# Kernel tuning notes

Hardware: AMD Instinct MI355X
Metric: run time of the kernel (lower is better)

## Reference

```python
import jax, jax.numpy as jnp
import numpy as np

EPS = 1e-8

def _cosine_weights(keys, M, reverse=False):
    # keys: (bs, r, W); M: (bs, W, N) -> softmax over slots of cosine sim, shape (bs, r, N)
    kn = keys / (jnp.linalg.norm(keys, axis=-1, keepdims=True) + EPS)
    Mn = M / (jnp.linalg.norm(M, axis=1, keepdims=True) + EPS)
    dist = jnp.einsum('brw,bwn->brn', kn, Mn)
    if reverse:
        dist = -dist
    return jax.nn.softmax(dist, axis=2)

def setup_inputs() -> dict:
    key = jax.random.key(0)
    ks = jax.random.split(key, 8)
    bs, W, N, R = 128, 256, 2048, 4
    return {
        'k_r': jax.random.normal(ks[0], (bs, R * W), jnp.float32),
        'm_t': jax.random.normal(ks[1], (bs, W), jnp.float32),
        'e_t': jax.random.normal(ks[2], (bs, W), jnp.float32),
        'm_erased': jax.random.normal(ks[3], (bs, 1, W), jnp.float32),
        'memory': jax.random.uniform(ks[4], (bs, W, N), jnp.float32),
        'gW': jax.random.normal(ks[5], (1, 2 * W), jnp.float32) * 0.05,
        'gb': jnp.zeros((1,), jnp.float32),
        'oW': jax.random.normal(ks[6], (W, 2 * W), jnp.float32) * 0.05,
        'ob': jnp.zeros((W,), jnp.float32),
    }

def reference(k_r, m_t, e_t, m_erased, memory, gW, gb, oW, ob):
    bs, W, N = memory.shape
    R = k_r.shape[1] // W
    read_keys = jnp.tanh(k_r.reshape(bs, R, W))
    write_m = jnp.tanh(m_t.reshape(bs, 1, W))            # m_t candidate (bs,1,W)
    erase_vec = jax.nn.softmax(e_t.reshape(bs, 1, W), axis=2)
    # MixGate(write_m, m_erased)
    cat = jnp.concatenate([write_m, m_erased], axis=-1)  # (bs,1,2W)
    g = jax.nn.sigmoid(jnp.einsum('biw,ow->bio', cat, gW) + gb)  # (bs,1,1)
    gated = jnp.concatenate([g * write_m, (1.0 - g) * m_erased], axis=-1)
    write_key = jax.nn.relu(jnp.einsum('biw,ow->bio', gated, oW) + ob)  # (bs,1,W)
    # content weighting with reversed (dissimilarity) cosine
    write_wt = _cosine_weights(write_key, memory, reverse=True)  # (bs,1,N)
    # M = M * (1 - et^T wt) + mt^T wt
    reset_gate = 1.0 - jnp.einsum('biw,bin->bwn', erase_vec, write_wt)
    M_new = memory * reset_gate + jnp.einsum('biw,bin->bwn', write_m, write_wt)
    # read
    read_wt = _cosine_weights(read_keys, M_new)          # (bs,R,N)
    m_read = jnp.einsum('brn,bwn->brw', read_wt, M_new)  # (bs,R,W)
    return (m_read, M_new, read_wt)
```

## Files before the change

kernel.cpp:

```cpp
#include <hip/hip_runtime.h>
#include <math.h>

#define EPS 1e-8f
#define BS 128
#define W 256
#define N 2048
#define R 4

using v4f = float __attribute__((ext_vector_type(4)));

__device__ inline float wave_sum(float v) {
#pragma unroll
    for (int o = 32; o > 0; o >>= 1) v += __shfl_xor(v, o, 64);
    return v;
}
__device__ inline float wave_max(float v) {
#pragma unroll
    for (int o = 32; o > 0; o >>= 1) v = fmaxf(v, __shfl_xor(v, o, 64));
    return v;
}

__global__ void k_prep(const float* __restrict__ k_r, const float* __restrict__ m_t,
                       const float* __restrict__ e_t, const float* __restrict__ m_er,
                       const float* __restrict__ gW, const float* __restrict__ gb,
                       const float* __restrict__ oW, const float* __restrict__ ob,
                       float* __restrict__ wm_o, float* __restrict__ er_o,
                       float* __restrict__ knw_o, float* __restrict__ knr_o) {
    int b = blockIdx.x, t = threadIdx.x;
    int lane = t & 63, wid = t >> 6;
    __shared__ float red[4];
    __shared__ float gated[2 * W];
    __shared__ float wk_s[W];

    float wm = tanhf(m_t[b * W + t]);
    float me = m_er[b * W + t];
    wm_o[b * W + t] = wm;

    float e = e_t[b * W + t];
    float mx = wave_max(e);
    if (lane == 0) red[wid] = mx;
    __syncthreads();
    mx = fmaxf(fmaxf(red[0], red[1]), fmaxf(red[2], red[3]));
    __syncthreads();
    float ex = expf(e - mx);
    float s = wave_sum(ex);
    if (lane == 0) red[wid] = s;
    __syncthreads();
    s = red[0] + red[1] + red[2] + red[3];
    __syncthreads();
    er_o[b * W + t] = ex / s;

    float p = wm * gW[t] + me * gW[W + t];
    float ps = wave_sum(p);
    if (lane == 0) red[wid] = ps;
    __syncthreads();
    ps = red[0] + red[1] + red[2] + red[3] + gb[0];
    __syncthreads();
    float g = 1.0f / (1.0f + expf(-ps));
    gated[t] = g * wm;
    gated[W + t] = (1.0f - g) * me;
    __syncthreads();

    const float4* g4 = (const float4*)gated;
    float4 g0 = g4[lane];
    float4 g1 = g4[64 + lane];
    for (int i = 0; i < 64; i++) {
        int o = wid * 64 + i;
        const float4* orow = (const float4*)(oW + (size_t)o * 2 * W);
        float4 w0 = orow[lane];
        float4 w1 = orow[64 + lane];
        float pp = w0.x * g0.x + w0.y * g0.y + w0.z * g0.z + w0.w * g0.w
                 + w1.x * g1.x + w1.y * g1.y + w1.z * g1.z + w1.w * g1.w;
        pp = wave_sum(pp);
        if (lane == 0) wk_s[o] = fmaxf(pp + ob[o], 0.0f);
    }
    __syncthreads();
    float wk = wk_s[t];
    float ss = wave_sum(wk * wk);
    if (lane == 0) red[wid] = ss;
    __syncthreads();
    ss = red[0] + red[1] + red[2] + red[3];
    __syncthreads();
    knw_o[b * W + t] = wk / (sqrtf(ss) + EPS);

    for (int r = 0; r < R; r++) {
        float rk = tanhf(k_r[(b * R + r) * W + t]);
        float s2 = wave_sum(rk * rk);
        if (lane == 0) red[wid] = s2;
        __syncthreads();
        s2 = red[0] + red[1] + red[2] + red[3];
        __syncthreads();
        knr_o[(b * R + r) * W + t] = rk / (sqrtf(s2) + EPS);
    }
}

__global__ void __launch_bounds__(256, 2)
k_wdist(const float* __restrict__ mem, const float* __restrict__ knw,
        float* __restrict__ dist) {
    int b = blockIdx.y;
    int t = threadIdx.x;
    int half = t >> 7, c = t & 127;
    int n4 = blockIdx.x * 128 + c;
    __shared__ float k[W];
    __shared__ float4 pdot[128], pss[128];
    k[t] = knw[b * W + t];
    __syncthreads();
    const float4* base = (const float4*)(mem + (size_t)b * W * N) + n4;
    float4 dot = make_float4(0.f, 0.f, 0.f, 0.f);
    float4 ss = make_float4(0.f, 0.f, 0.f, 0.f);
    int w0 = half * 128;
#pragma unroll 8
    for (int i = 0; i < 128; i++) {
        int w = w0 + i;
        float4 v = base[(size_t)w * (N / 4)];
        float kw = k[w];
        dot.x += kw * v.x; dot.y += kw * v.y; dot.z += kw * v.z; dot.w += kw * v.w;
        ss.x += v.x * v.x; ss.y += v.y * v.y; ss.z += v.z * v.z; ss.w += v.w * v.w;
    }
    if (half == 0) { pdot[c] = dot; pss[c] = ss; }
    __syncthreads();
    if (half == 1) {
        float4 od = pdot[c], os = pss[c];
        dot.x += od.x; dot.y += od.y; dot.z += od.z; dot.w += od.w;
        ss.x += os.x; ss.y += os.y; ss.z += os.z; ss.w += os.w;
        float4 o;
        o.x = -(dot.x / (sqrtf(ss.x) + EPS));
        o.y = -(dot.y / (sqrtf(ss.y) + EPS));
        o.z = -(dot.z / (sqrtf(ss.z) + EPS));
        o.w = -(dot.w / (sqrtf(ss.w) + EPS));
        ((float4*)(dist + (size_t)b * N))[n4] = o;
    }
}

__global__ void __launch_bounds__(256, 2)
k_update(const float* __restrict__ mem, const float* __restrict__ wdist,
         const float* __restrict__ er, const float* __restrict__ wm,
         const float* __restrict__ knr,
         float* __restrict__ Mnew, float* __restrict__ dist_raw) {
    int b = blockIdx.y;
    int t = threadIdx.x;
    int lane = t & 63, wid = t >> 6;
    int half = t >> 7, c = t & 127;
    int n4 = blockIdx.x * 128 + c;
    __shared__ float se[W], sw[W];
    __shared__ float4 skT[W];
    __shared__ float red[4];
    __shared__ float4 pd0[128], pd1[128], pd2[128], pd3[128], pssv[128];
    se[t] = er[b * W + t];
    sw[t] = wm[b * W + t];
    const float* kb = knr + (size_t)b * R * W;
    skT[t] = make_float4(kb[t], kb[W + t], kb[2 * W + t], kb[3 * W + t]);

    const float4* drow4 = (const float4*)(wdist + (size_t)b * N);
    float4 a0 = drow4[t];
    float4 a1 = drow4[256 + t];
    float mx = fmaxf(fmaxf(fmaxf(a0.x, a0.y), fmaxf(a0.z, a0.w)),
                     fmaxf(fmaxf(a1.x, a1.y), fmaxf(a1.z, a1.w)));
    mx = wave_max(mx);
    if (lane == 0) red[wid] = mx;
    __syncthreads();
    mx = fmaxf(fmaxf(red[0], red[1]), fmaxf(red[2], red[3]));
    __syncthreads();
    float sm = expf(a0.x - mx) + expf(a0.y - mx) + expf(a0.z - mx) + expf(a0.w - mx)
             + expf(a1.x - mx) + expf(a1.y - mx) + expf(a1.z - mx) + expf(a1.w - mx);
    sm = wave_sum(sm);
    if (lane == 0) red[wid] = sm;
    __syncthreads();
    sm = red[0] + red[1] + red[2] + red[3];
    float inv = 1.0f / sm;
    float4 dmine = drow4[n4];
    float4 wt;
    wt.x = expf(dmine.x - mx) * inv;
    wt.y = expf(dmine.y - mx) * inv;
    wt.z = expf(dmine.z - mx) * inv;
    wt.w = expf(dmine.w - mx) * inv;

    const float4* mb = (const float4*)(mem + (size_t)b * W * N) + n4;
    v4f* obv = (v4f*)(Mnew + (size_t)b * W * N) + n4;
    float4 ssv = make_float4(0.f, 0.f, 0.f, 0.f);
    float4 d0 = make_float4(0.f, 0.f, 0.f, 0.f);
    float4 d1 = make_float4(0.f, 0.f, 0.f, 0.f);
    float4 d2 = make_float4(0.f, 0.f, 0.f, 0.f);
    float4 d3 = make_float4(0.f, 0.f, 0.f, 0.f);
    int w0 = half * 128;
#pragma unroll 8
    for (int i = 0; i < 128; i++) {
        int w = w0 + i;
        float4 v = mb[(size_t)w * (N / 4)];
        float ew = se[w], mw = sw[w];
        float4 mn;
        mn.x = v.x + wt.x * (mw - v.x * ew);
        mn.y = v.y + wt.y * (mw - v.y * ew);
        mn.z = v.z + wt.z * (mw - v.z * ew);
        mn.w = v.w + wt.w * (mw - v.w * ew);
        v4f sv; sv[0] = mn.x; sv[1] = mn.y; sv[2] = mn.z; sv[3] = mn.w;
        __builtin_nontemporal_store(sv, obv + (size_t)w * (N / 4));
        ssv.x += mn.x * mn.x; ssv.y += mn.y * mn.y;
        ssv.z += mn.z * mn.z; ssv.w += mn.w * mn.w;
        float4 kv = skT[w];
        d0.x += kv.x * mn.x; d0.y += kv.x * mn.y; d0.z += kv.x * mn.z; d0.w += kv.x * mn.w;
        d1.x += kv.y * mn.x; d1.y += kv.y * mn.y; d1.z += kv.y * mn.z; d1.w += kv.y * mn.w;
        d2.x += kv.z * mn.x; d2.y += kv.z * mn.y; d2.z += kv.z * mn.z; d2.w += kv.z * mn.w;
        d3.x += kv.w * mn.x; d3.y += kv.w * mn.y; d3.z += kv.w * mn.z; d3.w += kv.w * mn.w;
    }
    if (half == 0) {
        pd0[c] = d0; pd1[c] = d1; pd2[c] = d2; pd3[c] = d3; pssv[c] = ssv;
    }
    __syncthreads();
    if (half == 1) {
        float4 q;
        q = pd0[c]; d0.x += q.x; d0.y += q.y; d0.z += q.z; d0.w += q.w;
        q = pd1[c]; d1.x += q.x; d1.y += q.y; d1.z += q.z; d1.w += q.w;
        q = pd2[c]; d2.x += q.x; d2.y += q.y; d2.z += q.z; d2.w += q.w;
        q = pd3[c]; d3.x += q.x; d3.y += q.y; d3.z += q.z; d3.w += q.w;
        q = pssv[c]; ssv.x += q.x; ssv.y += q.y; ssv.z += q.z; ssv.w += q.w;
        float4 ivn;
        ivn.x = 1.0f / (sqrtf(ssv.x) + EPS);
        ivn.y = 1.0f / (sqrtf(ssv.y) + EPS);
        ivn.z = 1.0f / (sqrtf(ssv.z) + EPS);
        ivn.w = 1.0f / (sqrtf(ssv.w) + EPS);
        float4* dr = (float4*)(dist_raw + (size_t)b * R * N);
        dr[0 * (N / 4) + n4] = make_float4(d0.x * ivn.x, d0.y * ivn.y, d0.z * ivn.z, d0.w * ivn.w);
        dr[1 * (N / 4) + n4] = make_float4(d1.x * ivn.x, d1.y * ivn.y, d1.z * ivn.z, d1.w * ivn.w);
        dr[2 * (N / 4) + n4] = make_float4(d2.x * ivn.x, d2.y * ivn.y, d2.z * ivn.z, d2.w * ivn.w);
        dr[3 * (N / 4) + n4] = make_float4(d3.x * ivn.x, d3.y * ivn.y, d3.z * ivn.z, d3.w * ivn.w);
    }
}

__global__ void __launch_bounds__(256, 2)
k_mread(const float* __restrict__ Mnew, const float* __restrict__ dist_raw,
        float* __restrict__ rwt_out, float* __restrict__ m_read) {
    int b = blockIdx.y;
    int w0 = blockIdx.x * 64;
    int t = threadIdx.x;
    int lane = t & 63, wid = t >> 6;

    __shared__ float rwt_s[R * N];
    __shared__ float redm[16], reds[16];
    __shared__ float part[64][2][4];

    const float4* drr = (const float4*)(dist_raw + (size_t)b * R * N);
    float4 a[R][2];
    float mxr[R], smr[R];
#pragma unroll
    for (int r = 0; r < R; r++) {
        a[r][0] = drr[r * 512 + t];
        a[r][1] = drr[r * 512 + 256 + t];
        float m0 = fmaxf(fmaxf(a[r][0].x, a[r][0].y), fmaxf(a[r][0].z, a[r][0].w));
        float m1 = fmaxf(fmaxf(a[r][1].x, a[r][1].y), fmaxf(a[r][1].z, a[r][1].w));
        float m = wave_max(fmaxf(m0, m1));
        if (lane == 0) redm[r * 4 + wid] = m;
    }
    __syncthreads();
#pragma unroll
    for (int r = 0; r < R; r++) {
        mxr[r] = fmaxf(fmaxf(redm[r * 4 + 0], redm[r * 4 + 1]),
                       fmaxf(redm[r * 4 + 2], redm[r * 4 + 3]));
        float4 e0, e1;
        e0.x = expf(a[r][0].x - mxr[r]); e0.y = expf(a[r][0].y - mxr[r]);
        e0.z = expf(a[r][0].z - mxr[r]); e0.w = expf(a[r][0].w - mxr[r]);
        e1.x = expf(a[r][1].x - mxr[r]); e1.y = expf(a[r][1].y - mxr[r]);
        e1.z = expf(a[r][1].z - mxr[r]); e1.w = expf(a[r][1].w - mxr[r]);
        a[r][0] = e0; a[r][1] = e1;
        float s = e0.x + e0.y + e0.z + e0.w + e1.x + e1.y + e1.z + e1.w;
        s = wave_sum(s);
        if (lane == 0) reds[r * 4 + wid] = s;
    }
    __syncthreads();
    float4* rs4 = (float4*)rwt_s;
#pragma unroll
    for (int r = 0; r < R; r++) {
        smr[r] = reds[r * 4 + 0] + reds[r * 4 + 1] + reds[r * 4 + 2] + reds[r * 4 + 3];
        float inv = 1.0f / smr[r];
        float4 o0, o1;
        o0.x = a[r][0].x * inv; o0.y = a[r][0].y * inv;
        o0.z = a[r][0].z * inv; o0.w = a[r][0].w * inv;
        o1.x = a[r][1].x * inv; o1.y = a[r][1].y * inv;
        o1.z = a[r][1].z * inv; o1.w = a[r][1].w * inv;
        rs4[r * 512 + t] = o0;
        rs4[r * 512 + 256 + t] = o1;
        if (blockIdx.x == 0) {
            float4* ro = (float4*)(rwt_out + (size_t)b * R * N);
            ro[r * 512 + t] = o0;
            ro[r * 512 + 256 + t] = o1;
        }
    }
    __syncthreads();

    int half = wid & 1, rowgrp = wid >> 1;
    int fbase = half * 256 + lane;

    float4 rw[R][4];
#pragma unroll
    for (int r = 0; r < R; r++)
#pragma unroll
        for (int k = 0; k < 4; k++) rw[r][k] = rs4[r * 512 + fbase + k * 64];

    const float* Mb = Mnew + (size_t)b * W * N;
#pragma unroll 4
    for (int wi = 0; wi < 32; wi++) {
        int wl = rowgrp * 32 + wi;
        const v4f* mrow = (const v4f*)(Mb + (size_t)(w0 + wl) * N);
        float4 v[4];
#pragma unroll
        for (int k = 0; k < 4; k++) {
            v4f vv = __builtin_nontemporal_load(mrow + fbase + k * 64);
            v[k].x = vv[0]; v[k].y = vv[1]; v[k].z = vv[2]; v[k].w = vv[3];
        }
        float a0 = 0.f, a1 = 0.f, a2 = 0.f, a3 = 0.f;
#pragma unroll
        for (int k = 0; k < 4; k++) {
            a0 += rw[0][k].x * v[k].x + rw[0][k].y * v[k].y + rw[0][k].z * v[k].z + rw[0][k].w * v[k].w;
            a1 += rw[1][k].x * v[k].x + rw[1][k].y * v[k].y + rw[1][k].z * v[k].z + rw[1][k].w * v[k].w;
            a2 += rw[2][k].x * v[k].x + rw[2][k].y * v[k].y + rw[2][k].z * v[k].z + rw[2][k].w * v[k].w;
            a3 += rw[3][k].x * v[k].x + rw[3][k].y * v[k].y + rw[3][k].z * v[k].z + rw[3][k].w * v[k].w;
        }
        a0 = wave_sum(a0);
        a1 = wave_sum(a1);
        a2 = wave_sum(a2);
        a3 = wave_sum(a3);
        if (lane == 0) {
            part[wl][half][0] = a0;
            part[wl][half][1] = a1;
            part[wl][half][2] = a2;
            part[wl][half][3] = a3;
        }
    }
    __syncthreads();
    int w = t >> 2, r = t & 3;
    float sres = part[w][0][r] + part[w][1][r];
    m_read[((size_t)b * R + r) * W + w0 + w] = sres;
}

extern "C" void kernel_launch(void* const* d_in, const int* in_sizes, int n_in,
                              void* d_out, int out_size, void* d_ws, size_t ws_size,
                              hipStream_t stream) {
    const float* k_r  = (const float*)d_in[0];
    const float* m_t  = (const float*)d_in[1];
    const float* e_t  = (const float*)d_in[2];
    const float* m_er = (const float*)d_in[3];
    const float* mem  = (const float*)d_in[4];
    const float* gW   = (const float*)d_in[5];
    const float* gb   = (const float*)d_in[6];
    const float* oW   = (const float*)d_in[7];
    const float* ob   = (const float*)d_in[8];

    float* out = (float*)d_out;
    float* m_read = out;
    float* Mnew   = out + (size_t)BS * R * W;
    float* rwt    = out + (size_t)BS * R * W + (size_t)BS * W * N;

    float* ws  = (float*)d_ws;
    float* wm  = ws;
    float* er  = ws + (size_t)BS * W;
    float* knw = ws + (size_t)2 * BS * W;
    float* knr = ws + (size_t)3 * BS * W;
    float* wdist = ws + (size_t)3 * BS * W + (size_t)BS * R * W;
    float* draw  = wdist + (size_t)BS * N;

    k_prep<<<BS, 256, 0, stream>>>(k_r, m_t, e_t, m_er, gW, gb, oW, ob, wm, er, knw, knr);
    k_wdist<<<dim3(4, BS), 256, 0, stream>>>(mem, knw, wdist);
    k_update<<<dim3(4, BS), 256, 0, stream>>>(mem, wdist, er, wm, knr, Mnew, draw);
    k_mread<<<dim3(4, BS), 256, 0, stream>>>(Mnew, draw, rwt, m_read);
}
```

Measured before the change: 250.4 us.

## Compute m_read from original memory via algebraic expansion of update

The read kernel now computes m_read from the original memory tensor rather than the freshly written Mnew. It uses the identity Mnew = M - er*(M·wt) + wm*wt and recomputes the write-weight softmax locally. This removes the kernel's dependence on Mnew but doubles the dot-product work and raises register and shared-memory use. Nontemporal loads are replaced with normal loads and the unroll factor is reduced.

```diff
diff --git a/kernel.cpp b/kernel.cpp
--- a/kernel.cpp
+++ b/kernel.cpp
@@ -228,7 +228,9 @@
 }
 
 __global__ void __launch_bounds__(256, 2)
-k_mread(const float* __restrict__ Mnew, const float* __restrict__ dist_raw,
+k_mread(const float* __restrict__ mem, const float* __restrict__ wdist_raw,
+        const float* __restrict__ dist_raw, const float* __restrict__ er_g,
+        const float* __restrict__ wm_g,
         float* __restrict__ rwt_out, float* __restrict__ m_read) {
     int b = blockIdx.y;
     int w0 = blockIdx.x * 64;
@@ -236,100 +238,127 @@
     int lane = t & 63, wid = t >> 6;
 
     __shared__ float rwt_s[R * N];
-    __shared__ float redm[16], reds[16];
-    __shared__ float part[64][2][4];
+    __shared__ float u_s[R * N];
+    __shared__ float redm[20], reds[20], redc[16];
+    __shared__ float part_a[64][2][4], part_b[64][2][4];
 
     const float4* drr = (const float4*)(dist_raw + (size_t)b * R * N);
-    float4 a[R][2];
-    float mxr[R], smr[R];
+    const float4* dw4 = (const float4*)(wdist_raw + (size_t)b * N);
+    float4 a[5][2];
 #pragma unroll
     for (int r = 0; r < R; r++) {
         a[r][0] = drr[r * 512 + t];
         a[r][1] = drr[r * 512 + 256 + t];
-        float m0 = fmaxf(fmaxf(a[r][0].x, a[r][0].y), fmaxf(a[r][0].z, a[r][0].w));
-        float m1 = fmaxf(fmaxf(a[r][1].x, a[r][1].y), fmaxf(a[r][1].z, a[r][1].w));
+    }
+    a[4][0] = dw4[t];
+    a[4][1] = dw4[256 + t];
+#pragma unroll
+    for (int i = 0; i < 5; i++) {
+        float m0 = fmaxf(fmaxf(a[i][0].x, a[i][0].y), fmaxf(a[i][0].z, a[i][0].w));
+        float m1 = fmaxf(fmaxf(a[i][1].x, a[i][1].y), fmaxf(a[i][1].z, a[i][1].w));
         float m = wave_max(fmaxf(m0, m1));
-        if (lane == 0) redm[r * 4 + wid] = m;
-    }
-    __syncthreads();
-#pragma unroll
-    for (int r = 0; r < R; r++) {
-        mxr[r] = fmaxf(fmaxf(redm[r * 4 + 0], redm[r * 4 + 1]),
-                       fmaxf(redm[r * 4 + 2], redm[r * 4 + 3]));
+        if (lane == 0) redm[i * 4 + wid] = m;
+    }
+    __syncthreads();
+#pragma unroll
+    for (int i = 0; i < 5; i++) {
+        float mx = fmaxf(fmaxf(redm[i * 4 + 0], redm[i * 4 + 1]),
+                         fmaxf(redm[i * 4 + 2], redm[i * 4 + 3]));
         float4 e0, e1;
-        e0.x = expf(a[r][0].x - mxr[r]); e0.y = expf(a[r][0].y - mxr[r]);
-        e0.z = expf(a[r][0].z - mxr[r]); e0.w = expf(a[r][0].w - mxr[r]);
-        e1.x = expf(a[r][1].x - mxr[r]); e1.y = expf(a[r][1].y - mxr[r]);
-        e1.z = expf(a[r][1].z - mxr[r]); e1.w = expf(a[r][1].w - mxr[r]);
-        a[r][0] = e0; a[r][1] = e1;
+        e0.x = expf(a[i][0].x - mx); e0.y = expf(a[i][0].y - mx);
+        e0.z = expf(a[i][0].z - mx); e0.w = expf(a[i][0].w - mx);
+        e1.x = expf(a[i][1].x - mx); e1.y = expf(a[i][1].y - mx);
+        e1.z = expf(a[i][1].z - mx); e1.w = expf(a[i][1].w - mx);
+        a[i][0] = e0; a[i][1] = e1;
         float s = e0.x + e0.y + e0.z + e0.w + e1.x + e1.y + e1.z + e1.w;
         s = wave_sum(s);
-        if (lane == 0) reds[r * 4 + wid] = s;
-    }
-    __syncthreads();
+        if (lane == 0) reds[i * 4 + wid] = s;
+    }
+    __syncthreads();
+    float invw = 1.0f / (reds[16] + reds[17] + reds[18] + reds[19]);
+    float4 wt0, wt1;
+    wt0.x = a[4][0].x * invw; wt0.y = a[4][0].y * invw;
+    wt0.z = a[4][0].z * invw; wt0.w = a[4][0].w * invw;
+    wt1.x = a[4][1].x * invw; wt1.y = a[4][1].y * invw;
+    wt1.z = a[4][1].z * invw; wt1.w = a[4][1].w * invw;
+
     float4* rs4 = (float4*)rwt_s;
+    float4* us4 = (float4*)u_s;
 #pragma unroll
     for (int r = 0; r < R; r++) {
-        smr[r] = reds[r * 4 + 0] + reds[r * 4 + 1] + reds[r * 4 + 2] + reds[r * 4 + 3];
-        float inv = 1.0f / smr[r];
-        float4 o0, o1;
+        float inv = 1.0f / (reds[r * 4 + 0] + reds[r * 4 + 1] + reds[r * 4 + 2] + reds[r * 4 + 3]);
+        float4 o0, o1, u0, u1;
         o0.x = a[r][0].x * inv; o0.y = a[r][0].y * inv;
         o0.z = a[r][0].z * inv; o0.w = a[r][0].w * inv;
         o1.x = a[r][1].x * inv; o1.y = a[r][1].y * inv;
         o1.z = a[r][1].z * inv; o1.w = a[r][1].w * inv;
+        u0.x = o0.x * wt0.x; u0.y = o0.y * wt0.y; u0.z = o0.z * wt0.z; u0.w = o0.w * wt0.w;
+        u1.x = o1.x * wt1.x; u1.y = o1.y * wt1.y; u1.z = o1.z * wt1.z; u1.w = o1.w * wt1.w;
         rs4[r * 512 + t] = o0;
         rs4[r * 512 + 256 + t] = o1;
+        us4[r * 512 + t] = u0;
+        us4[r * 512 + 256 + t] = u1;
         if (blockIdx.x == 0) {
             float4* ro = (float4*)(rwt_out + (size_t)b * R * N);
             ro[r * 512 + t] = o0;
             ro[r * 512 + 256 + t] = o1;
         }
+        float cp = u0.x + u0.y + u0.z + u0.w + u1.x + u1.y + u1.z + u1.w;
+        cp = wave_sum(cp);
+        if (lane == 0) redc[r * 4 + wid] = cp;
     }
     __syncthreads();
 
     int half = wid & 1, rowgrp = wid >> 1;
     int fbase = half * 256 + lane;
 
-    float4 rw[R][4];
+    float4 rw[R][4], uw[R][4];
 #pragma unroll
     for (int r = 0; r < R; r++)
 #pragma unroll
-        for (int k = 0; k < 4; k++) rw[r][k] = rs4[r * 512 + fbase + k * 64];
-
-    const float* Mb = Mnew + (size_t)b * W * N;
-#pragma unroll 4
+        for (int k = 0; k < 4; k++) {
+            rw[r][k] = rs4[r * 512 + fbase + k * 64];
+            uw[r][k] = us4[r * 512 + fbase + k * 64];
+        }
+
+    const float* Mb = mem + (size_t)b * W * N;
+#pragma unroll 2
     for (int wi = 0; wi < 32; wi++) {
         int wl = rowgrp * 32 + wi;
-        const v4f* mrow = (const v4f*)(Mb + (size_t)(w0 + wl) * N);
+        const float4* mrow = (const float4*)(Mb + (size_t)(w0 + wl) * N);
         float4 v[4];
 #pragma unroll
-        for (int k = 0; k < 4; k++) {
-            v4f vv = __builtin_nontemporal_load(mrow + fbase + k * 64);
-            v[k].x = vv[0]; v[k].y = vv[1]; v[k].z = vv[2]; v[k].w = vv[3];
-        }
+        for (int k = 0; k < 4; k++) v[k] = mrow[fbase + k * 64];
         float a0 = 0.f, a1 = 0.f, a2 = 0.f, a3 = 0.f;
+        float b0 = 0.f, b1 = 0.f, b2 = 0.f, b3 = 0.f;
 #pragma unroll
         for (int k = 0; k < 4; k++) {
             a0 += rw[0][k].x * v[k].x + rw[0][k].y * v[k].y + rw[0][k].z * v[k].z + rw[0][k].w * v[k].w;
             a1 += rw[1][k].x * v[k].x + rw[1][k].y * v[k].y + rw[1][k].z * v[k].z + rw[1][k].w * v[k].w;
             a2 += rw[2][k].x * v[k].x + rw[2][k].y * v[k].y + rw[2][k].z * v[k].z + rw[2][k].w * v[k].w;
             a3 += rw[3][k].x * v[k].x + rw[3][k].y * v[k].y + rw[3][k].z * v[k].z + rw[3][k].w * v[k].w;
+            b0 += uw[0][k].x * v[k].x + uw[0][k].y * v[k].y + uw[0][k].z * v[k].z + uw[0][k].w * v[k].w;
+            b1 += uw[1][k].x * v[k].x + uw[1][k].y * v[k].y + uw[1][k].z * v[k].z + uw[1][k].w * v[k].w;
+            b2 += uw[2][k].x * v[k].x + uw[2][k].y * v[k].y + uw[2][k].z * v[k].z + uw[2][k].w * v[k].w;
+            b3 += uw[3][k].x * v[k].x + uw[3][k].y * v[k].y + uw[3][k].z * v[k].z + uw[3][k].w * v[k].w;
         }
-        a0 = wave_sum(a0);
-        a1 = wave_sum(a1);
-        a2 = wave_sum(a2);
-        a3 = wave_sum(a3);
+        a0 = wave_sum(a0); a1 = wave_sum(a1); a2 = wave_sum(a2); a3 = wave_sum(a3);
+        b0 = wave_sum(b0); b1 = wave_sum(b1); b2 = wave_sum(b2); b3 = wave_sum(b3);
         if (lane == 0) {
-            part[wl][half][0] = a0;
-            part[wl][half][1] = a1;
-            part[wl][half][2] = a2;
-            part[wl][half][3] = a3;
+            part_a[wl][half][0] = a0; part_a[wl][half][1] = a1;
+            part_a[wl][half][2] = a2; part_a[wl][half][3] = a3;
+            part_b[wl][half][0] = b0; part_b[wl][half][1] = b1;
+            part_b[wl][half][2] = b2; part_b[wl][half][3] = b3;
         }
     }
     __syncthreads();
     int w = t >> 2, r = t & 3;
-    float sres = part[w][0][r] + part[w][1][r];
-    m_read[((size_t)b * R + r) * W + w0 + w] = sres;
+    float A = part_a[w][0][r] + part_a[w][1][r];
+    float B = part_b[w][0][r] + part_b[w][1][r];
+    float C = redc[r * 4 + 0] + redc[r * 4 + 1] + redc[r * 4 + 2] + redc[r * 4 + 3];
+    float erv = er_g[b * W + w0 + w];
+    float wmv = wm_g[b * W + w0 + w];
+    m_read[((size_t)b * R + r) * W + w0 + w] = A - erv * B + wmv * C;
 }
 
 extern "C" void kernel_launch(void* const* d_in, const int* in_sizes, int n_in,
@@ -361,5 +390,5 @@
     k_prep<<<BS, 256, 0, stream>>>(k_r, m_t, e_t, m_er, gW, gb, oW, ob, wm, er, knw, knr);
     k_wdist<<<dim3(4, BS), 256, 0, stream>>>(mem, knw, wdist);
     k_update<<<dim3(4, BS), 256, 0, stream>>>(mem, wdist, er, wm, knr, Mnew, draw);
-    k_mread<<<dim3(4, BS), 256, 0, stream>>>(Mnew, draw, rwt, m_read);
-}
+    k_mread<<<dim3(4, BS), 256, 0, stream>>>(mem, wdist, draw, er, wm, rwt, m_read);
+}
```

Measured after the change: 251.6 us. About the same (+0.5%).
